# Kernel tuning notes

Hardware: AMD Instinct MI355X
Metric: run time of the kernel (lower is better)

The kernel has to match this reference:

```python
import jax, jax.numpy as jnp
import numpy as np

NUM_HEADS = 8

def setup_inputs() -> dict:
    key = jax.random.key(0)
    ks = jax.random.split(key, 5)
    B, N, D = 2, 2048, 512
    x = jax.random.normal(ks[0], (B, N, D), dtype=jnp.float32)
    qkv_w = jax.random.normal(ks[1], (3 * D, D), dtype=jnp.float32) * (D ** -0.5)
    qkv_b = jax.random.normal(ks[2], (3 * D,), dtype=jnp.float32) * 0.02
    proj_w = jax.random.normal(ks[3], (D, D), dtype=jnp.float32) * (D ** -0.5)
    proj_b = jax.random.normal(ks[4], (D,), dtype=jnp.float32) * 0.02
    return {"x": x, "qkv_w": qkv_w, "qkv_b": qkv_b, "proj_w": proj_w, "proj_b": proj_b}

def reference(x, qkv_w, qkv_b, proj_w, proj_b):
    B, N, D = x.shape
    H = NUM_HEADS
    hd = D // H
    scale = hd ** -0.5
    # qkv projection: [B,N,3D] -> [B,N,3,H,hd]
    qkv = (jnp.einsum('bnd,ed->bne', x, qkv_w) + qkv_b).reshape(B, N, 3, H, hd)
    q, k, v = qkv[:, :, 0], qkv[:, :, 1], qkv[:, :, 2]
    q = q * scale
    attn = jnp.einsum('bnhd,bmhd->bhnm', q, k)  # [B,H,N,M]
    # L2-normalize each score row before softmax (the custom modification)
    attn = attn / (jnp.linalg.norm(attn, axis=-1, keepdims=True) + 1e-6)
    attn = jax.nn.softmax(attn, axis=-1)
    out = jnp.einsum('bhnm,bmhd->bnhd', attn, v).reshape(B, N, D)
    return jnp.einsum('bnd,ed->bne', out, proj_w) + proj_b
```

## Files before the change

kernel.cpp:

```cpp
#include <hip/hip_runtime.h>
#include <hip/hip_bf16.h>
#include <cstdint>

typedef __attribute__((ext_vector_type(8))) short short8;
typedef __attribute__((ext_vector_type(4))) float floatx4;

__device__ __forceinline__ float bf2f(unsigned short u) {
  union { unsigned int i; float f; } v;
  v.i = ((unsigned int)u) << 16;
  return v.f;
}
__device__ __forceinline__ unsigned short f2bf(float f) {
  union { float f; unsigned int i; } v; v.f = f;
  unsigned int r = v.i + 0x7FFFu + ((v.i >> 16) & 1u);
  return (unsigned short)(r >> 16);
}

__device__ __forceinline__ void async_copy16(const void* g, void* l) {
  __builtin_amdgcn_global_load_lds(
      (const __attribute__((address_space(1))) void*)g,
      (__attribute__((address_space(3))) void*)l, 16, 0, 0);
}

__global__ __launch_bounds__(256) void convert3_kernel(
    const float* __restrict__ x, const float* __restrict__ w1,
    const float* __restrict__ w2, unsigned short* __restrict__ xb,
    unsigned short* __restrict__ w1b, unsigned short* __restrict__ w2b) {
  constexpr int N0 = 4096 * 512 / 8, N1 = 1536 * 512 / 8, N2 = 512 * 512 / 8;
  int i = blockIdx.x * 256 + threadIdx.x;
  const float* src;
  unsigned short* dst;
  int off;
  if (i < N0) { src = x; dst = xb; off = i; }
  else if (i < N0 + N1) { src = w1; dst = w1b; off = i - N0; }
  else if (i < N0 + N1 + N2) { src = w2; dst = w2b; off = i - N0 - N1; }
  else return;
  const float4* p = (const float4*)src + (size_t)off * 2;
  float4 a = p[0], b = p[1];
  short8 r;
  r[0] = (short)f2bf(a.x); r[1] = (short)f2bf(a.y);
  r[2] = (short)f2bf(a.z); r[3] = (short)f2bf(a.w);
  r[4] = (short)f2bf(b.x); r[5] = (short)f2bf(b.y);
  r[6] = (short)f2bf(b.z); r[7] = (short)f2bf(b.w);
  *(short8*)(dst + (size_t)off * 8) = r;
}

template <int BM, int BN, typename OutT>
__global__ __launch_bounds__(256) void gemm_tiled_kernel(
    const unsigned short* __restrict__ A, const unsigned short* __restrict__ W,
    const float* __restrict__ bias, OutT* __restrict__ out,
    int M, int N, int K) {
  constexpr int BK = 64;
  constexpr int MI = BM / 32;
  constexpr int NI = BN / 32;
  __shared__ __align__(16) unsigned short As[BM * BK];
  __shared__ __align__(16) unsigned short Ws[BN * BK];

  int tid = threadIdx.x, wave = tid >> 6, lane = tid & 63;
  int l16 = lane & 15, quad = lane >> 4;
  int bm = blockIdx.x, bn = blockIdx.y;
  int wm = (wave & 1) * (BM / 2), wn = (wave >> 1) * (BN / 2);

  floatx4 acc[MI][NI] = {};

  for (int kk = 0; kk < K; kk += BK) {
    __syncthreads();
#pragma unroll
    for (int c = 0; c < MI; c++) {
      int ci = (wave * MI + c) * 64 + lane;
      int row = ci >> 3, col8 = (ci & 7) ^ (row & 7);
      async_copy16(A + (size_t)(bm * BM + row) * K + kk + col8 * 8,
                   As + (size_t)ci * 8);
    }
#pragma unroll
    for (int c = 0; c < NI; c++) {
      int ci = (wave * NI + c) * 64 + lane;
      int row = ci >> 3, col8 = (ci & 7) ^ (row & 7);
      async_copy16(W + (size_t)(bn * BN + row) * K + kk + col8 * 8,
                   Ws + (size_t)ci * 8);
    }
    __syncthreads();

#pragma unroll
    for (int k2 = 0; k2 < 2; k2++) {
      short8 a[MI], w8[NI];
#pragma unroll
      for (int mi = 0; mi < MI; mi++) {
        int row = wm + mi * 16 + l16;
        int slot = ((k2 * 4 + quad) ^ (row & 7));
        a[mi] = *(const short8*)(As + row * 64 + slot * 8);
      }
#pragma unroll
      for (int ni = 0; ni < NI; ni++) {
        int row = wn + ni * 16 + l16;
        int slot = ((k2 * 4 + quad) ^ (row & 7));
        w8[ni] = *(const short8*)(Ws + row * 64 + slot * 8);
      }
#pragma unroll
      for (int mi = 0; mi < MI; mi++)
#pragma unroll
        for (int ni = 0; ni < NI; ni++)
          acc[mi][ni] = __builtin_amdgcn_mfma_f32_16x16x32_bf16(
              a[mi], w8[ni], acc[mi][ni], 0, 0, 0);
    }
  }

#pragma unroll
  for (int ni = 0; ni < NI; ni++) {
    int col = bn * BN + wn + ni * 16 + l16;
    float bb = bias[col];
#pragma unroll
    for (int mi = 0; mi < MI; mi++) {
#pragma unroll
      for (int r = 0; r < 4; r++) {
        int row = bm * BM + wm + mi * 16 + quad * 4 + r;
        float v = acc[mi][ni][r] + bb;
        if constexpr (sizeof(OutT) == 2)
          out[(size_t)row * N + col] = (OutT)f2bf(v);
        else
          out[(size_t)row * N + col] = (OutT)v;
      }
    }
  }
}

__global__ __launch_bounds__(256) void kv_transpose_kernel(
    const unsigned short* __restrict__ qkv, unsigned short* __restrict__ kt,
    unsigned short* __restrict__ vt) {
  __shared__ __align__(16) unsigned short TK[64 * 72];
  __shared__ __align__(16) unsigned short TV[64 * 72];
  int nb = blockIdx.x, bh = blockIdx.y;
  int b = bh >> 3, h = bh & 7;
  int t = threadIdx.x;
#pragma unroll
  for (int c = 0; c < 2; c++) {
    int ci = c * 256 + t;
    int row = ci >> 3, ch = ci & 7;
    const unsigned short* src =
        qkv + (size_t)(b * 2048 + nb * 64 + row) * 1536 + h * 64 + ch * 8;
    *(short8*)(TK + row * 72 + ch * 8) = *(const short8*)(src + 512);
    *(short8*)(TV + row * 72 + ch * 8) = *(const short8*)(src + 1024);
  }
  __syncthreads();
  int d = t & 63, nblk = t >> 6;
  short8 k0, k1, v0, v1;
#pragma unroll
  for (int i = 0; i < 8; i++) {
    k0[i] = (short)TK[(nblk * 16 + i) * 72 + d];
    k1[i] = (short)TK[(nblk * 16 + 8 + i) * 72 + d];
    v0[i] = (short)TV[(nblk * 16 + i) * 72 + d];
    v1[i] = (short)TV[(nblk * 16 + 8 + i) * 72 + d];
  }
  size_t orow = ((size_t)bh * 64 + d) * 2048 + nb * 64 + nblk * 16;
  *(short8*)(kt + orow) = k0;
  *(short8*)(kt + orow + 8) = k1;
  *(short8*)(vt + orow) = v0;
  *(short8*)(vt + orow + 8) = v1;
}

__global__ __launch_bounds__(256) void g_partial_kernel(
    const unsigned short* __restrict__ kt, float* __restrict__ gpart) {
  int bh = blockIdx.x, sl = blockIdx.y;
  int tid = threadIdx.x, wave = tid >> 6, lane = tid & 63;
  int l16 = lane & 15, quad = lane >> 4;
  const unsigned short* kb = kt + (size_t)bh * 64 * 2048;

  floatx4 acc[4] = {};
  for (int ks = 0; ks < 8; ks++) {
    int k0 = sl * 256 + ks * 32 + quad * 8;
    short8 a = *(const short8*)(kb + (size_t)(wave * 16 + l16) * 2048 + k0);
#pragma unroll
    for (int dt = 0; dt < 4; dt++) {
      short8 bb = *(const short8*)(kb + (size_t)(dt * 16 + l16) * 2048 + k0);
      acc[dt] = __builtin_amdgcn_mfma_f32_16x16x32_bf16(a, bb, acc[dt], 0, 0, 0);
    }
  }
  float* gout = gpart + ((size_t)(bh * 8 + sl)) * 4096;
#pragma unroll
  for (int dt = 0; dt < 4; dt++)
#pragma unroll
    for (int r = 0; r < 4; r++)
      gout[(wave * 16 + quad * 4 + r) * 64 + dt * 16 + l16] = acc[dt][r];
}

__global__ __launch_bounds__(256) void g_reduce_kernel(
    const float* __restrict__ gpart, unsigned short* __restrict__ gb) {
  int i = blockIdx.x * 256 + threadIdx.x;
  int bh = i >> 12, ed = i & 4095;
  const float* p = gpart + (size_t)(bh * 8) * 4096 + ed;
  float s = 0.f;
#pragma unroll
  for (int j = 0; j < 8; j++) s += p[j * 4096];
  gb[i] = f2bf(s);
}

__global__ __launch_bounds__(256, 4) void attn_kernel(
    const unsigned short* __restrict__ qkv,
    const unsigned short* __restrict__ vt,
    const unsigned short* __restrict__ gb,
    unsigned short* __restrict__ attn_out) {
  constexpr int NSEQ = 2048, LD = 1536, DM = 512;
  const float scale = 0.125f;

  __shared__ __align__(16) unsigned short Kb[128 * 64];
  __shared__ __align__(16) unsigned short Vtb[64 * 128];
  __shared__ __align__(16) unsigned short Pb[32 * 128];

  int qb = blockIdx.x, h = blockIdx.y, b = blockIdx.z;
  int tid = threadIdx.x, wave = tid >> 6, lane = tid & 63;
  int l16 = lane & 15, quad = lane >> 4;

  const unsigned short* base = qkv + (size_t)b * NSEQ * LD;
  const unsigned short* vbase = vt + (size_t)(b * 8 + h) * 64 * NSEQ;

  short8 aq[2][2];
#pragma unroll
  for (int mi = 0; mi < 2; mi++) {
    const unsigned short* qp =
        base + (size_t)(qb * 32 + mi * 16 + l16) * LD + h * 64;
    aq[mi][0] = *(const short8*)(qp + quad * 8);
    aq[mi][1] = *(const short8*)(qp + 32 + quad * 8);
  }

  const unsigned short* gbh = gb + (size_t)(b * 8 + h) * 4096;
  float sumsq[2][4] = {};
#pragma unroll
  for (int eti = 0; eti < 4; eti++) {
    floatx4 t[2] = {};
#pragma unroll
    for (int k2 = 0; k2 < 2; k2++) {
      short8 bg = *(const short8*)(gbh + (eti * 16 + l16) * 64 + k2 * 32 + quad * 8);
#pragma unroll
      for (int mi = 0; mi < 2; mi++)
        t[mi] = __builtin_amdgcn_mfma_f32_16x16x32_bf16(aq[mi][k2], bg, t[mi], 0, 0, 0);
    }
#pragma unroll
    for (int mi = 0; mi < 2; mi++)
#pragma unroll
      for (int r = 0; r < 4; r++) {
        float qv = bf2f(base[(size_t)(qb * 32 + mi * 16 + quad * 4 + r) * LD +
                             h * 64 + eti * 16 + l16]);
        sumsq[mi][r] += t[mi][r] * qv;
      }
  }
  float invk[2][4];
#pragma unroll
  for (int mi = 0; mi < 2; mi++)
#pragma unroll
    for (int r = 0; r < 4; r++) {
#pragma unroll
      for (int m = 1; m <= 8; m <<= 1)
        sumsq[mi][r] += __shfl_xor(sumsq[mi][r], m, 64);
      invk[mi][r] = scale / (scale * sqrtf(sumsq[mi][r]) + 1e-6f);
    }

  floatx4 o[2] = {};
  float lsum[2][4] = {};

  for (int mc = 0; mc < NSEQ; mc += 128) {
    __syncthreads();
#pragma unroll
    for (int c = 0; c < 4; c++) {
      int ci = (wave * 4 + c) * 64 + lane;
      int row = ci >> 3, sc = (ci & 7) ^ (row & 7);
      async_copy16(base + (size_t)(mc + row) * LD + 512 + h * 64 + sc * 8,
                   Kb + (size_t)ci * 8);
    }
#pragma unroll
    for (int c = 0; c < 4; c++) {
      int ci = (wave * 4 + c) * 64 + lane;
      int d = ci >> 4, sc = (ci & 15) ^ (d & 15);
      async_copy16(vbase + (size_t)d * NSEQ + mc + sc * 8,
                   Vtb + (size_t)ci * 8);
    }
    __syncthreads();

#pragma unroll
    for (int st = 0; st < 2; st++) {
      int row = wave * 32 + st * 16 + l16;
      floatx4 s[2] = {};
#pragma unroll
      for (int k2 = 0; k2 < 2; k2++) {
        short8 bk = *(const short8*)(Kb + row * 64 +
                                     (((k2 * 4 + quad) ^ (row & 7)) * 8));
#pragma unroll
        for (int mi = 0; mi < 2; mi++)
          s[mi] = __builtin_amdgcn_mfma_f32_16x16x32_bf16(aq[mi][k2], bk, s[mi], 0, 0, 0);
      }
      int kvc = wave * 4 + st * 2 + (l16 >> 3);
#pragma unroll
      for (int mi = 0; mi < 2; mi++)
#pragma unroll
        for (int r = 0; r < 4; r++) {
          float p = __expf(s[mi][r] * invk[mi][r]);
          lsum[mi][r] += p;
          int q = mi * 16 + quad * 4 + r;
          Pb[q * 128 + ((kvc ^ (q & 15)) << 3) + (l16 & 7)] = f2bf(p);
        }
    }
    __syncthreads();

    int d = wave * 16 + l16;
#pragma unroll
    for (int ks = 0; ks < 4; ks++) {
      short8 bv = *(const short8*)(Vtb + d * 128 + (((ks * 4 + quad) ^ l16) * 8));
#pragma unroll
      for (int mi = 0; mi < 2; mi++) {
        int q = mi * 16 + l16;
        short8 ap = *(const short8*)(Pb + q * 128 + (((ks * 4 + quad) ^ (q & 15)) << 3));
        o[mi] = __builtin_amdgcn_mfma_f32_16x16x32_bf16(ap, bv, o[mi], 0, 0, 0);
      }
    }
  }
  __syncthreads();

#pragma unroll
  for (int mi = 0; mi < 2; mi++)
#pragma unroll
    for (int r = 0; r < 4; r++)
#pragma unroll
      for (int m = 1; m <= 8; m <<= 1)
        lsum[mi][r] += __shfl_xor(lsum[mi][r], m, 64);
  float* Red = (float*)Pb;
  if (l16 == 0) {
#pragma unroll
    for (int mi = 0; mi < 2; mi++)
#pragma unroll
      for (int r = 0; r < 4; r++)
        Red[wave * 32 + mi * 16 + quad * 4 + r] = lsum[mi][r];
  }
  __syncthreads();

  size_t ob = ((size_t)b * NSEQ + qb * 32) * DM + h * 64 + wave * 16 + l16;
#pragma unroll
  for (int mi = 0; mi < 2; mi++)
#pragma unroll
    for (int r = 0; r < 4; r++) {
      int q = mi * 16 + quad * 4 + r;
      float tot = Red[q] + Red[32 + q] + Red[64 + q] + Red[96 + q];
      attn_out[ob + (size_t)q * DM] = f2bf(o[mi][r] / tot);
    }
}

extern "C" void kernel_launch(void* const* d_in, const int* in_sizes, int n_in,
                              void* d_out, int out_size, void* d_ws, size_t ws_size,
                              hipStream_t stream) {
  const float* x = (const float*)d_in[0];
  const float* qkv_w = (const float*)d_in[1];
  const float* qkv_b = (const float*)d_in[2];
  const float* proj_w = (const float*)d_in[3];
  const float* proj_b = (const float*)d_in[4];
  float* out = (float*)d_out;

  unsigned short* xb = (unsigned short*)d_ws;
  unsigned short* qkvw_b = xb + (size_t)4096 * 512;
  unsigned short* projw_b = qkvw_b + (size_t)1536 * 512;
  unsigned short* qkv = projw_b + (size_t)512 * 512;
  unsigned short* attn_out = qkv + (size_t)4096 * 1536;
  unsigned short* vt = attn_out + (size_t)4096 * 512;
  unsigned short* gbuf = vt + (size_t)16 * 64 * 2048;
  unsigned short* kt = xb;
  float* gpart = (float*)attn_out;

  convert3_kernel<<<1536, 256, 0, stream>>>(x, qkv_w, proj_w, xb, qkvw_b, projw_b);
  gemm_tiled_kernel<128, 64, unsigned short>
      <<<dim3(4096 / 128, 1536 / 64), 256, 0, stream>>>(
          xb, qkvw_b, qkv_b, qkv, 4096, 1536, 512);
  kv_transpose_kernel<<<dim3(32, 16), 256, 0, stream>>>(qkv, kt, vt);
  g_partial_kernel<<<dim3(16, 8), 256, 0, stream>>>(kt, gpart);
  g_reduce_kernel<<<256, 256, 0, stream>>>(gpart, gbuf);
  attn_kernel<<<dim3(64, 8, 2), 256, 0, stream>>>(qkv, vt, gbuf, attn_out);
  gemm_tiled_kernel<64, 64, float>
      <<<dim3(4096 / 64, 512 / 64), 256, 0, stream>>>(
          attn_out, projw_b, proj_b, out, 4096, 512, 512);
}
```

Baseline: 150.7 us.

## Fuse K/V transpose into QKV GEMM epilogue and stream K/V via registers in attention

The QKV GEMM epilogue now writes transposed K and V directly into kt/vt buffers, which removes the separate kv_transpose kernel and its extra read/write pass over K and V. The attention kernel drops its LDS staging of K and V tiles. Each wave instead loads its own K rows and V^T slices from global memory into registers, prefetching the next chunk while the current one is computed. The cost is more register pressure and uncoalesced 8-byte transposed stores in the GEMM epilogue. Workspace aliasing of kt and gpart is also swapped to fit the new lifetimes.

```diff
diff --git a/kernel.cpp b/kernel.cpp
--- a/kernel.cpp
+++ b/kernel.cpp
@@ -3,6 +3,7 @@
 #include <cstdint>
 
 typedef __attribute__((ext_vector_type(8))) short short8;
+typedef __attribute__((ext_vector_type(4))) short bfx4;
 typedef __attribute__((ext_vector_type(4))) float floatx4;
 
 __device__ __forceinline__ float bf2f(unsigned short u) {
@@ -45,11 +46,12 @@
   *(short8*)(dst + (size_t)off * 8) = r;
 }
 
-template <int BM, int BN, typename OutT>
+template <int BM, int BN, typename OutT, bool FUSE_KV>
 __global__ __launch_bounds__(256) void gemm_tiled_kernel(
     const unsigned short* __restrict__ A, const unsigned short* __restrict__ W,
     const float* __restrict__ bias, OutT* __restrict__ out,
-    int M, int N, int K) {
+    int M, int N, int K,
+    unsigned short* __restrict__ kt, unsigned short* __restrict__ vt) {
   constexpr int BK = 64;
   constexpr int MI = BM / 32;
   constexpr int NI = BN / 32;
@@ -105,57 +107,45 @@
     }
   }
 
+  int sec = 0, hh = 0;
+  if constexpr (FUSE_KV) { sec = bn >> 3; hh = bn & 7; }
+
 #pragma unroll
   for (int ni = 0; ni < NI; ni++) {
     int col = bn * BN + wn + ni * 16 + l16;
     float bb = bias[col];
 #pragma unroll
     for (int mi = 0; mi < MI; mi++) {
-#pragma unroll
-      for (int r = 0; r < 4; r++) {
-        int row = bm * BM + wm + mi * 16 + quad * 4 + r;
-        float v = acc[mi][ni][r] + bb;
-        if constexpr (sizeof(OutT) == 2)
-          out[(size_t)row * N + col] = (OutT)f2bf(v);
-        else
-          out[(size_t)row * N + col] = (OutT)v;
-      }
-    }
-  }
-}
-
-__global__ __launch_bounds__(256) void kv_transpose_kernel(
-    const unsigned short* __restrict__ qkv, unsigned short* __restrict__ kt,
-    unsigned short* __restrict__ vt) {
-  __shared__ __align__(16) unsigned short TK[64 * 72];
-  __shared__ __align__(16) unsigned short TV[64 * 72];
-  int nb = blockIdx.x, bh = blockIdx.y;
-  int b = bh >> 3, h = bh & 7;
-  int t = threadIdx.x;
-#pragma unroll
-  for (int c = 0; c < 2; c++) {
-    int ci = c * 256 + t;
-    int row = ci >> 3, ch = ci & 7;
-    const unsigned short* src =
-        qkv + (size_t)(b * 2048 + nb * 64 + row) * 1536 + h * 64 + ch * 8;
-    *(short8*)(TK + row * 72 + ch * 8) = *(const short8*)(src + 512);
-    *(short8*)(TV + row * 72 + ch * 8) = *(const short8*)(src + 1024);
-  }
-  __syncthreads();
-  int d = t & 63, nblk = t >> 6;
-  short8 k0, k1, v0, v1;
-#pragma unroll
-  for (int i = 0; i < 8; i++) {
-    k0[i] = (short)TK[(nblk * 16 + i) * 72 + d];
-    k1[i] = (short)TK[(nblk * 16 + 8 + i) * 72 + d];
-    v0[i] = (short)TV[(nblk * 16 + i) * 72 + d];
-    v1[i] = (short)TV[(nblk * 16 + 8 + i) * 72 + d];
-  }
-  size_t orow = ((size_t)bh * 64 + d) * 2048 + nb * 64 + nblk * 16;
-  *(short8*)(kt + orow) = k0;
-  *(short8*)(kt + orow + 8) = k1;
-  *(short8*)(vt + orow) = v0;
-  *(short8*)(vt + orow + 8) = v1;
+      float v[4];
+#pragma unroll
+      for (int r = 0; r < 4; r++) v[r] = acc[mi][ni][r] + bb;
+      int row0 = bm * BM + wm + mi * 16 + quad * 4;
+      if constexpr (FUSE_KV) {
+        if (sec >= 1) {
+          bfx4 pk;
+#pragma unroll
+          for (int r = 0; r < 4; r++) pk[r] = (short)f2bf(v[r]);
+          int d = col & 63;
+          int bidx = row0 >> 11, n0 = row0 & 2047;
+          unsigned short* dst = (sec == 1) ? kt : vt;
+          *(bfx4*)(dst + ((size_t)((bidx * 8 + hh) * 64 + d)) * 2048 + n0) = pk;
+        }
+        if (sec <= 1) {
+#pragma unroll
+          for (int r = 0; r < 4; r++)
+            out[(size_t)(row0 + r) * N + col] = (OutT)f2bf(v[r]);
+        }
+      } else {
+#pragma unroll
+        for (int r = 0; r < 4; r++) {
+          if constexpr (sizeof(OutT) == 2)
+            out[(size_t)(row0 + r) * N + col] = (OutT)f2bf(v[r]);
+          else
+            out[(size_t)(row0 + r) * N + col] = (OutT)v[r];
+        }
+      }
+    }
+  }
 }
 
 __global__ __launch_bounds__(256) void g_partial_kernel(
@@ -202,8 +192,6 @@
   constexpr int NSEQ = 2048, LD = 1536, DM = 512;
   const float scale = 0.125f;
 
-  __shared__ __align__(16) unsigned short Kb[128 * 64];
-  __shared__ __align__(16) unsigned short Vtb[64 * 128];
   __shared__ __align__(16) unsigned short Pb[32 * 128];
 
   int qb = blockIdx.x, h = blockIdx.y, b = blockIdx.z;
@@ -254,39 +242,44 @@
       invk[mi][r] = scale / (scale * sqrtf(sumsq[mi][r]) + 1e-6f);
     }
 
+  const unsigned short* kp0 =
+      base + (size_t)(wave * 32 + l16) * LD + 512 + h * 64 + quad * 8;
+  const unsigned short* vp0 = vbase + (size_t)(wave * 16 + l16) * NSEQ + quad * 8;
+
   floatx4 o[2] = {};
   float lsum[2][4] = {};
 
+  short8 bk[4], bv[4], nbk[4], nbv[4];
+#pragma unroll
+  for (int st = 0; st < 2; st++)
+#pragma unroll
+    for (int k2 = 0; k2 < 2; k2++)
+      bk[st * 2 + k2] = *(const short8*)(kp0 + (size_t)st * 16 * LD + k2 * 32);
+#pragma unroll
+  for (int ks = 0; ks < 4; ks++) bv[ks] = *(const short8*)(vp0 + ks * 32);
+
   for (int mc = 0; mc < NSEQ; mc += 128) {
-    __syncthreads();
-#pragma unroll
-    for (int c = 0; c < 4; c++) {
-      int ci = (wave * 4 + c) * 64 + lane;
-      int row = ci >> 3, sc = (ci & 7) ^ (row & 7);
-      async_copy16(base + (size_t)(mc + row) * LD + 512 + h * 64 + sc * 8,
-                   Kb + (size_t)ci * 8);
-    }
-#pragma unroll
-    for (int c = 0; c < 4; c++) {
-      int ci = (wave * 4 + c) * 64 + lane;
-      int d = ci >> 4, sc = (ci & 15) ^ (d & 15);
-      async_copy16(vbase + (size_t)d * NSEQ + mc + sc * 8,
-                   Vtb + (size_t)ci * 8);
-    }
-    __syncthreads();
+    if (mc + 128 < NSEQ) {
+      const unsigned short* kp = kp0 + (size_t)(mc + 128) * LD;
+      const unsigned short* vp = vp0 + mc + 128;
+#pragma unroll
+      for (int st = 0; st < 2; st++)
+#pragma unroll
+        for (int k2 = 0; k2 < 2; k2++)
+          nbk[st * 2 + k2] = *(const short8*)(kp + (size_t)st * 16 * LD + k2 * 32);
+#pragma unroll
+      for (int ks = 0; ks < 4; ks++) nbv[ks] = *(const short8*)(vp + ks * 32);
+    }
 
 #pragma unroll
     for (int st = 0; st < 2; st++) {
-      int row = wave * 32 + st * 16 + l16;
       floatx4 s[2] = {};
 #pragma unroll
-      for (int k2 = 0; k2 < 2; k2++) {
-        short8 bk = *(const short8*)(Kb + row * 64 +
-                                     (((k2 * 4 + quad) ^ (row & 7)) * 8));
+      for (int k2 = 0; k2 < 2; k2++)
 #pragma unroll
         for (int mi = 0; mi < 2; mi++)
-          s[mi] = __builtin_amdgcn_mfma_f32_16x16x32_bf16(aq[mi][k2], bk, s[mi], 0, 0, 0);
-      }
+          s[mi] = __builtin_amdgcn_mfma_f32_16x16x32_bf16(
+              aq[mi][k2], bk[st * 2 + k2], s[mi], 0, 0, 0);
       int kvc = wave * 4 + st * 2 + (l16 >> 3);
 #pragma unroll
       for (int mi = 0; mi < 2; mi++)
@@ -300,19 +293,21 @@
     }
     __syncthreads();
 
-    int d = wave * 16 + l16;
 #pragma unroll
     for (int ks = 0; ks < 4; ks++) {
-      short8 bv = *(const short8*)(Vtb + d * 128 + (((ks * 4 + quad) ^ l16) * 8));
 #pragma unroll
       for (int mi = 0; mi < 2; mi++) {
         int q = mi * 16 + l16;
-        short8 ap = *(const short8*)(Pb + q * 128 + (((ks * 4 + quad) ^ (q & 15)) << 3));
-        o[mi] = __builtin_amdgcn_mfma_f32_16x16x32_bf16(ap, bv, o[mi], 0, 0, 0);
-      }
-    }
-  }
-  __syncthreads();
+        short8 ap = *(const short8*)(Pb + q * 128 +
+                                     (((ks * 4 + quad) ^ (q & 15)) << 3));
+        o[mi] = __builtin_amdgcn_mfma_f32_16x16x32_bf16(ap, bv[ks], o[mi], 0, 0, 0);
+      }
+    }
+    __syncthreads();
+
+#pragma unroll
+    for (int i = 0; i < 4; i++) { bk[i] = nbk[i]; bv[i] = nbv[i]; }
+  }
 
 #pragma unroll
   for (int mi = 0; mi < 2; mi++)
@@ -359,18 +354,17 @@
   unsigned short* attn_out = qkv + (size_t)4096 * 1536;
   unsigned short* vt = attn_out + (size_t)4096 * 512;
   unsigned short* gbuf = vt + (size_t)16 * 64 * 2048;
-  unsigned short* kt = xb;
-  float* gpart = (float*)attn_out;
+  unsigned short* kt = attn_out;
+  float* gpart = (float*)xb;
 
   convert3_kernel<<<1536, 256, 0, stream>>>(x, qkv_w, proj_w, xb, qkvw_b, projw_b);
-  gemm_tiled_kernel<128, 64, unsigned short>
+  gemm_tiled_kernel<128, 64, unsigned short, true>
       <<<dim3(4096 / 128, 1536 / 64), 256, 0, stream>>>(
-          xb, qkvw_b, qkv_b, qkv, 4096, 1536, 512);
-  kv_transpose_kernel<<<dim3(32, 16), 256, 0, stream>>>(qkv, kt, vt);
+          xb, qkvw_b, qkv_b, qkv, 4096, 1536, 512, kt, vt);
   g_partial_kernel<<<dim3(16, 8), 256, 0, stream>>>(kt, gpart);
   g_reduce_kernel<<<256, 256, 0, stream>>>(gpart, gbuf);
   attn_kernel<<<dim3(64, 8, 2), 256, 0, stream>>>(qkv, vt, gbuf, attn_out);
-  gemm_tiled_kernel<64, 64, float>
+  gemm_tiled_kernel<64, 64, float, false>
       <<<dim3(4096 / 64, 512 / 64), 256, 0, stream>>>(
-          attn_out, projw_b, proj_b, out, 4096, 512, 512);
-}
+          attn_out, projw_b, proj_b, out, 4096, 512, 512, nullptr, nullptr);
+}
```

Result: slower. 200.9 us (+33.3%).
